# Kernel tuning notes

Hardware: AMD Instinct MI355X
Metric: run time of the kernel (lower is better)

Reference implementation:

```python
import jax, jax.numpy as jnp
import numpy as np

EPS = 1e-6

def layernorm2d(x, w, b):
    # normalize over channel dim (axis=1) of NCHW, per spatial location
    mu = jnp.mean(x, axis=1, keepdims=True)
    var = jnp.var(x, axis=1, keepdims=True)
    xn = (x - mu) * jax.lax.rsqrt(var + EPS)
    return xn * w[None, :, None, None] + b[None, :, None, None]

def conv1x1(x, w, b):
    # x: (B,C,H,W), w: (O,C), b: (O,)
    return jnp.einsum('bchw,oc->bohw', x, w) + b[None, :, None, None]

def setup_inputs() -> dict:
    key = jax.random.key(0)
    ks = jax.random.split(key, 9)
    B, C, H, W = 8, 256, 128, 128
    scale = 1.0 / np.sqrt(C)
    return {
        'x': jax.random.normal(ks[0], (B, C, H, W), jnp.float32),
        'norm_w': jnp.ones((C,), jnp.float32),
        'norm_b': jnp.zeros((C,), jnp.float32),
        'wq': jax.random.normal(ks[1], (C, C), jnp.float32) * scale,
        'bq': jnp.zeros((C,), jnp.float32),
        'wk': jax.random.normal(ks[2], (C, C), jnp.float32) * scale,
        'bk': jnp.zeros((C,), jnp.float32),
        'wv': jax.random.normal(ks[3], (C, C), jnp.float32) * scale,
        'bv': jnp.zeros((C,), jnp.float32),
        'beta': jax.random.normal(ks[4], (1, C, 1, 1), jnp.float32) * 0.1,
    }

def reference(x, norm_w, norm_b, wq, bq, wk, bk, wv, bv, beta):
    C = x.shape[1]
    scale = C ** (-0.5)
    xn = layernorm2d(x, norm_w, norm_b)
    Q = conv1x1(xn, wq, bq)          # (B,C,H,W)
    K = conv1x1(xn, wk, bk)          # (B,C,H,W)
    V = conv1x1(x, wv, bv)           # (B,C,H,W)
    # axial (per-row) attention: logits (B,H,W,W)
    attn = jnp.einsum('bchw,bchv->bhwv', Q, K) * scale
    A = jax.nn.softmax(attn, axis=-1)
    F_self = jnp.einsum('bhwv,bchv->bchw', A, V)
    return x + F_self * beta
```

## Files before the change

### kernel.cpp

```cpp
#include <hip/hip_runtime.h>
#include <hip/hip_bf16.h>

typedef short short8 __attribute__((ext_vector_type(8)));
typedef float f32x4 __attribute__((ext_vector_type(4)));

#define LDS_BYTES 163840
#define XS 0
#define XN 65536
#define AT 65536
#define YT 98304
#define GB 131072
#define SUMSO 139264
#define SQSO 141312
#define MUO 143360
#define RSO 143872
#define UDO 144384

__device__ inline unsigned short cvtbf(float f){
  unsigned int x = __float_as_uint(f);
  x += 0x7fffu + ((x >> 16) & 1u);
  return (unsigned short)(x >> 16);
}
__device__ inline float bf2f(unsigned short u){ return __uint_as_float(((unsigned int)u) << 16); }
__device__ inline unsigned int pk2(float a, float b){ return (unsigned int)cvtbf(a) | ((unsigned int)cvtbf(b) << 16); }

__global__ void __launch_bounds__(256) setup_kernel(
    const float* __restrict__ wq, const float* __restrict__ bq,
    const float* __restrict__ wk, const float* __restrict__ wvw,
    unsigned short* __restrict__ Mbf, unsigned short* __restrict__ wvbf, float* __restrict__ u){
  int c1 = blockIdx.x, t = threadIdx.x;
  float acc = 0.f;
  for (int o = 0; o < 256; ++o) acc = fmaf(wq[o*256 + c1], wk[o*256 + t], acc);
  Mbf[c1*256 + t] = cvtbf(acc);
  wvbf[c1*256 + t] = cvtbf(wvw[c1*256 + t]);
  if (c1 == 0){
    float a2 = 0.f;
    for (int o = 0; o < 256; ++o) a2 = fmaf(wk[o*256 + t], bq[o], a2);
    u[t] = a2;
  }
}

__global__ void __launch_bounds__(512, 2) fused_kernel(
    const float* __restrict__ x, const float* __restrict__ nw, const float* __restrict__ nb,
    const float* __restrict__ bvv, const float* __restrict__ beta,
    const unsigned short* __restrict__ Mbf, const unsigned short* __restrict__ wvbf,
    const float* __restrict__ u, float* __restrict__ out){
  extern __shared__ char smem[];
  const int t = threadIdx.x;
  const int lane = t & 63, wv8 = t >> 6;
  const int g = lane >> 4, li = lane & 15;
  const int blk = blockIdx.x;
  const int b = blk >> 7, h = blk & 127;
  const size_t base = (size_t)b*4194304 + (size_t)h*128;

  #pragma unroll
  for (int i = 0; i < 16; ++i){
    int f = t + i*512;
    int c = f >> 5, w4 = f & 31;
    const float4 v = *(const float4*)(x + base + (size_t)c*16384 + (size_t)(w4*4));
    uint2 p; p.x = pk2(v.x, v.y); p.y = pk2(v.z, v.w);
    *(uint2*)(smem + XS + c*256 + ((w4*8) ^ ((c&7)<<4))) = p;
  }
  __syncthreads();

  {
    int w = t & 127, s = t >> 7;
    float sm = 0.f, sq = 0.f;
    for (int j = 0; j < 64; ++j){
      int c = s*64 + j;
      float xv = bf2f(*(const unsigned short*)(smem + XS + c*256 + ((2*w) ^ ((c&7)<<4))));
      sm += xv; sq += xv*xv;
    }
    ((float*)(smem + SUMSO))[s*128 + w] = sm;
    ((float*)(smem + SQSO))[s*128 + w] = sq;
  }
  __syncthreads();
  if (t < 128){
    float sm = 0.f, sq = 0.f;
    for (int s = 0; s < 4; ++s){ sm += ((float*)(smem+SUMSO))[s*128+t]; sq += ((float*)(smem+SQSO))[s*128+t]; }
    float mu = sm * (1.f/256.f);
    float var = sq * (1.f/256.f) - mu*mu;
    ((float*)(smem+MUO))[t] = mu;
    ((float*)(smem+RSO))[t] = rsqrtf(var + 1e-6f);
  }
  __syncthreads();

  {
    int w = t & 127, s = t >> 7;
    float mu = ((float*)(smem+MUO))[w], rs = ((float*)(smem+RSO))[w];
    float ud = 0.f;
    for (int i = 0; i < 8; ++i){
      int c0 = s*64 + i*8;
      short8 o8;
      #pragma unroll
      for (int j = 0; j < 8; ++j){
        int c = c0 + j;
        float xv = bf2f(*(const unsigned short*)(smem + XS + c*256 + ((2*w) ^ ((c&7)<<4))));
        float xnv = (xv - mu)*rs*nw[c] + nb[c];
        o8[j] = (short)cvtbf(xnv);
        ud = fmaf(u[c], xnv, ud);
      }
      *(short8*)(smem + XN + w*512 + ((2*c0) ^ ((w&7)<<4))) = o8;
    }
    ((float*)(smem+SUMSO))[s*128 + w] = ud;
  }
  __syncthreads();
  if (t < 128){
    float ud = 0.f; for (int s = 0; s < 4; ++s) ud += ((float*)(smem+SUMSO))[s*128+t];
    ((float*)(smem+UDO))[t] = ud;
  }
  __syncthreads();

  f32x4 Sacc[8];
  #pragma unroll
  for (int vt = 0; vt < 8; ++vt){
    int vb = vt*16 + g*4;
    #pragma unroll
    for (int r = 0; r < 4; ++r) Sacc[vt][r] = ((float*)(smem+UDO))[vb + r];
  }
  const int ot = wv8 >> 2, vp = wv8 & 3;
  const int wt = wv8;
  for (int k8 = 0; k8 < 8; ++k8){
    f32x4 Ga[2] = {{0.f,0.f,0.f,0.f},{0.f,0.f,0.f,0.f}};
    #pragma unroll
    for (int kk = 0; kk < 8; ++kk){
      int o = k8*32 + ot*16 + li;
      short8 afr = *(const short8*)(Mbf + o*256 + kk*32 + g*8);
      #pragma unroll
      for (int j = 0; j < 2; ++j){
        int v = (vp*2 + j)*16 + li;
        short8 bfr = *(const short8*)(smem + XN + v*512 + ((2*(kk*32 + g*8)) ^ ((v&7)<<4)));
        Ga[j] = __builtin_amdgcn_mfma_f32_16x16x32_bf16(afr, bfr, Ga[j], 0, 0, 0);
      }
    }
    __syncthreads();
    #pragma unroll
    for (int j = 0; j < 2; ++j){
      int v = (vp*2 + j)*16 + li;
      int ob = ot*16 + g*4;
      uint2 p; p.x = pk2(Ga[j][0], Ga[j][1]); p.y = pk2(Ga[j][2], Ga[j][3]);
      *(uint2*)(smem + GB + v*64 + ((2*ob) ^ ((v&3)<<4))) = p;
    }
    __syncthreads();
    {
      int w = wt*16 + li;
      short8 bfr = *(const short8*)(smem + XN + w*512 + ((2*(k8*32 + g*8)) ^ ((w&7)<<4)));
      #pragma unroll
      for (int vt = 0; vt < 8; ++vt){
        int v = vt*16 + li;
        short8 afr = *(const short8*)(smem + GB + v*64 + ((16*g) ^ ((v&3)<<4)));
        Sacc[vt] = __builtin_amdgcn_mfma_f32_16x16x32_bf16(afr, bfr, Sacc[vt], 0, 0, 0);
      }
    }
  }
  __syncthreads();

  float mx = -3.4e38f;
  #pragma unroll
  for (int vt = 0; vt < 8; ++vt)
    #pragma unroll
    for (int r = 0; r < 4; ++r){ float sv = Sacc[vt][r]*0.0625f; Sacc[vt][r] = sv; mx = fmaxf(mx, sv); }
  mx = fmaxf(mx, __shfl_xor(mx, 16));
  mx = fmaxf(mx, __shfl_xor(mx, 32));
  float sum = 0.f;
  #pragma unroll
  for (int vt = 0; vt < 8; ++vt)
    #pragma unroll
    for (int r = 0; r < 4; ++r){ float p = exp2f((Sacc[vt][r]-mx)*1.44269504f); Sacc[vt][r] = p; sum += p; }
  sum += __shfl_xor(sum, 16);
  sum += __shfl_xor(sum, 32);
  float inv = 1.f / sum;
  {
    int w = wt*16 + li;
    #pragma unroll
    for (int vt = 0; vt < 8; ++vt){
      uint2 p; p.x = pk2(Sacc[vt][0]*inv, Sacc[vt][1]*inv); p.y = pk2(Sacc[vt][2]*inv, Sacc[vt][3]*inv);
      int vb = vt*16 + g*4;
      *(uint2*)(smem + AT + w*256 + ((2*vb) ^ ((w&7)<<4))) = p;
    }
  }
  __syncthreads();

  f32x4 Yacc[2][8];
  #pragma unroll
  for (int ci = 0; ci < 2; ++ci)
    #pragma unroll
    for (int w2 = 0; w2 < 8; ++w2) Yacc[ci][w2] = (f32x4){0.f,0.f,0.f,0.f};
  #pragma unroll
  for (int kk = 0; kk < 4; ++kk){
    short8 afr[2];
    #pragma unroll
    for (int ci = 0; ci < 2; ++ci){
      int c = (wv8*2 + ci)*16 + li;
      afr[ci] = *(const short8*)(smem + XS + c*256 + ((2*(kk*32 + g*8)) ^ ((c&7)<<4)));
    }
    #pragma unroll
    for (int w2 = 0; w2 < 8; ++w2){
      int w = w2*16 + li;
      short8 bfr = *(const short8*)(smem + AT + w*256 + ((2*(kk*32 + g*8)) ^ ((w&7)<<4)));
      #pragma unroll
      for (int ci = 0; ci < 2; ++ci)
        Yacc[ci][w2] = __builtin_amdgcn_mfma_f32_16x16x32_bf16(afr[ci], bfr, Yacc[ci][w2], 0, 0, 0);
    }
  }
  #pragma unroll
  for (int ci = 0; ci < 2; ++ci){
    int cb = (wv8*2 + ci)*16 + g*4;
    #pragma unroll
    for (int w2 = 0; w2 < 8; ++w2){
      int w = w2*16 + li;
      uint2 p; p.x = pk2(Yacc[ci][w2][0], Yacc[ci][w2][1]); p.y = pk2(Yacc[ci][w2][2], Yacc[ci][w2][3]);
      *(uint2*)(smem + YT + w*512 + ((2*cb) ^ ((w&7)<<4))) = p;
    }
  }
  __syncthreads();

  f32x4 Facc[2][8];
  #pragma unroll
  for (int oi = 0; oi < 2; ++oi)
    #pragma unroll
    for (int w2 = 0; w2 < 8; ++w2) Facc[oi][w2] = (f32x4){0.f,0.f,0.f,0.f};
  #pragma unroll
  for (int kk = 0; kk < 8; ++kk){
    short8 afr[2];
    #pragma unroll
    for (int oi = 0; oi < 2; ++oi){
      int o = (wv8*2 + oi)*16 + li;
      afr[oi] = *(const short8*)(wvbf + o*256 + kk*32 + g*8);
    }
    #pragma unroll
    for (int w2 = 0; w2 < 8; ++w2){
      int w = w2*16 + li;
      short8 bfr = *(const short8*)(smem + YT + w*512 + ((2*(kk*32 + g*8)) ^ ((w&7)<<4)));
      #pragma unroll
      for (int oi = 0; oi < 2; ++oi)
        Facc[oi][w2] = __builtin_amdgcn_mfma_f32_16x16x32_bf16(afr[oi], bfr, Facc[oi][w2], 0, 0, 0);
    }
  }
  #pragma unroll
  for (int oi = 0; oi < 2; ++oi){
    #pragma unroll
    for (int r = 0; r < 4; ++r){
      int o = (wv8*2 + oi)*16 + g*4 + r;
      float bvo = bvv[o], bto = beta[o];
      #pragma unroll
      for (int w2 = 0; w2 < 8; ++w2){
        int w = w2*16 + li;
        size_t idx = base + (size_t)o*16384 + (size_t)w;
        out[idx] = x[idx] + (Facc[oi][w2][r] + bvo)*bto;
      }
    }
  }
}

extern "C" void kernel_launch(void* const* d_in, const int* in_sizes, int n_in,
                              void* d_out, int out_size, void* d_ws, size_t ws_size,
                              hipStream_t stream) {
  (void)in_sizes; (void)n_in; (void)out_size; (void)ws_size;
  const float* x      = (const float*)d_in[0];
  const float* norm_w = (const float*)d_in[1];
  const float* norm_b = (const float*)d_in[2];
  const float* wq     = (const float*)d_in[3];
  const float* bq     = (const float*)d_in[4];
  const float* wk     = (const float*)d_in[5];
  const float* wvw    = (const float*)d_in[7];
  const float* bvv    = (const float*)d_in[8];
  const float* beta   = (const float*)d_in[9];
  float* out = (float*)d_out;

  unsigned short* Mbf  = (unsigned short*)d_ws;
  unsigned short* wvbf = (unsigned short*)((char*)d_ws + 131072);
  float* u             = (float*)((char*)d_ws + 262144);

  static bool attr_set = false;
  if (!attr_set) {
    (void)hipFuncSetAttribute((const void*)fused_kernel,
                              hipFuncAttributeMaxDynamicSharedMemorySize, LDS_BYTES);
    attr_set = true;
  }

  setup_kernel<<<256, 256, 0, stream>>>(wq, bq, wk, wvw, Mbf, wvbf, u);
  fused_kernel<<<1024, 512, LDS_BYTES, stream>>>(x, norm_w, norm_b, bvv, beta, Mbf, wvbf, u, out);
}
```

Measured before the change: 192.1 us.

## Shrink LDS footprint by dropping x tile and splitting Y staging in halves

Removes the bf16 copy of x from shared memory: layernorm statistics are computed straight from global loads, with x kept in registers as packed bf16, and the V-projection operand is reloaded from global/L2 and converted on the fly. The Y intermediate is staged in two channel halves that reuse a smaller buffer, cutting LDS from about 160KB to about 78KB. Launch bounds are raised to allow 4 blocks per CU. The setup kernel now computes four rows per block. The cost is higher register pressure (32 packed registers plus the accumulators), repeated global reads of x, and extra barriers from the two-half staging.

```diff
diff --git a/kernel.cpp b/kernel.cpp
--- a/kernel.cpp
+++ b/kernel.cpp
@@ -4,17 +4,16 @@
 typedef short short8 __attribute__((ext_vector_type(8)));
 typedef float f32x4 __attribute__((ext_vector_type(4)));
 
-#define LDS_BYTES 163840
-#define XS 0
-#define XN 65536
-#define AT 65536
-#define YT 98304
-#define GB 131072
-#define SUMSO 139264
-#define SQSO 141312
-#define MUO 143360
-#define RSO 143872
-#define UDO 144384
+#define XN 0
+#define AT 0
+#define YTH 32768
+#define GB 65536
+#define SUMO 73728
+#define SQO 75776
+#define MUO 77824
+#define RSO 78336
+#define UDO 78848
+#define LDS_BYTES 79360
 
 __device__ inline unsigned short cvtbf(float f){
   unsigned int x = __float_as_uint(f);
@@ -28,20 +27,28 @@
     const float* __restrict__ wq, const float* __restrict__ bq,
     const float* __restrict__ wk, const float* __restrict__ wvw,
     unsigned short* __restrict__ Mbf, unsigned short* __restrict__ wvbf, float* __restrict__ u){
-  int c1 = blockIdx.x, t = threadIdx.x;
-  float acc = 0.f;
-  for (int o = 0; o < 256; ++o) acc = fmaf(wq[o*256 + c1], wk[o*256 + t], acc);
-  Mbf[c1*256 + t] = cvtbf(acc);
-  wvbf[c1*256 + t] = cvtbf(wvw[c1*256 + t]);
-  if (c1 == 0){
+  int t = threadIdx.x;
+  int c1b = blockIdx.x * 4;
+  float acc[4] = {0.f,0.f,0.f,0.f};
+  for (int o = 0; o < 256; ++o){
+    float wkv = wk[o*256 + t];
+    #pragma unroll
+    for (int i = 0; i < 4; ++i) acc[i] = fmaf(wq[o*256 + c1b + i], wkv, acc[i]);
+  }
+  #pragma unroll
+  for (int i = 0; i < 4; ++i){
+    Mbf[(c1b+i)*256 + t] = cvtbf(acc[i]);
+    wvbf[(c1b+i)*256 + t] = cvtbf(wvw[(c1b+i)*256 + t]);
+  }
+  if (blockIdx.x == 0){
     float a2 = 0.f;
     for (int o = 0; o < 256; ++o) a2 = fmaf(wk[o*256 + t], bq[o], a2);
     u[t] = a2;
   }
 }
 
-__global__ void __launch_bounds__(512, 2) fused_kernel(
-    const float* __restrict__ x, const float* __restrict__ nw, const float* __restrict__ nb,
+__global__ void __launch_bounds__(512, 4) fused_kernel(
+    const float* __restrict__ x, const float* __restrict__ nw, const float* __restrict__ nbp,
     const float* __restrict__ bvv, const float* __restrict__ beta,
     const unsigned short* __restrict__ Mbf, const unsigned short* __restrict__ wvbf,
     const float* __restrict__ u, float* __restrict__ out){
@@ -53,31 +60,26 @@
   const int b = blk >> 7, h = blk & 127;
   const size_t base = (size_t)b*4194304 + (size_t)h*128;
 
-  #pragma unroll
-  for (int i = 0; i < 16; ++i){
-    int f = t + i*512;
-    int c = f >> 5, w4 = f & 31;
-    const float4 v = *(const float4*)(x + base + (size_t)c*16384 + (size_t)(w4*4));
-    uint2 p; p.x = pk2(v.x, v.y); p.y = pk2(v.z, v.w);
-    *(uint2*)(smem + XS + c*256 + ((w4*8) ^ ((c&7)<<4))) = p;
-  }
-  __syncthreads();
-
+  const int w = t & 127, s = t >> 7;
+  unsigned int xp[32];
   {
-    int w = t & 127, s = t >> 7;
+    const float* xw = x + base + (size_t)(s*64)*16384 + w;
     float sm = 0.f, sq = 0.f;
-    for (int j = 0; j < 64; ++j){
-      int c = s*64 + j;
-      float xv = bf2f(*(const unsigned short*)(smem + XS + c*256 + ((2*w) ^ ((c&7)<<4))));
-      sm += xv; sq += xv*xv;
-    }
-    ((float*)(smem + SUMSO))[s*128 + w] = sm;
-    ((float*)(smem + SQSO))[s*128 + w] = sq;
+    #pragma unroll
+    for (int j = 0; j < 32; ++j){
+      float a0 = xw[(size_t)(2*j)*16384];
+      float a1 = xw[(size_t)(2*j+1)*16384];
+      sm += a0 + a1;
+      sq = fmaf(a0, a0, sq); sq = fmaf(a1, a1, sq);
+      xp[j] = pk2(a0, a1);
+    }
+    ((float*)(smem + SUMO))[s*128 + w] = sm;
+    ((float*)(smem + SQO))[s*128 + w] = sq;
   }
   __syncthreads();
   if (t < 128){
     float sm = 0.f, sq = 0.f;
-    for (int s = 0; s < 4; ++s){ sm += ((float*)(smem+SUMSO))[s*128+t]; sq += ((float*)(smem+SQSO))[s*128+t]; }
+    for (int q = 0; q < 4; ++q){ sm += ((float*)(smem+SUMO))[q*128+t]; sq += ((float*)(smem+SQO))[q*128+t]; }
     float mu = sm * (1.f/256.f);
     float var = sq * (1.f/256.f) - mu*mu;
     ((float*)(smem+MUO))[t] = mu;
@@ -86,27 +88,31 @@
   __syncthreads();
 
   {
-    int w = t & 127, s = t >> 7;
     float mu = ((float*)(smem+MUO))[w], rs = ((float*)(smem+RSO))[w];
     float ud = 0.f;
+    #pragma unroll
     for (int i = 0; i < 8; ++i){
       int c0 = s*64 + i*8;
       short8 o8;
       #pragma unroll
-      for (int j = 0; j < 8; ++j){
-        int c = c0 + j;
-        float xv = bf2f(*(const unsigned short*)(smem + XS + c*256 + ((2*w) ^ ((c&7)<<4))));
-        float xnv = (xv - mu)*rs*nw[c] + nb[c];
-        o8[j] = (short)cvtbf(xnv);
-        ud = fmaf(u[c], xnv, ud);
+      for (int j = 0; j < 4; ++j){
+        unsigned int p = xp[i*4 + j];
+        int c = c0 + j*2;
+        float xa = bf2f((unsigned short)(p & 0xffffu));
+        float xb = bf2f((unsigned short)(p >> 16));
+        float na = (xa - mu)*rs*nw[c]   + nbp[c];
+        float nbv = (xb - mu)*rs*nw[c+1] + nbp[c+1];
+        ud = fmaf(u[c], na, fmaf(u[c+1], nbv, ud));
+        o8[j*2]   = (short)cvtbf(na);
+        o8[j*2+1] = (short)cvtbf(nbv);
       }
       *(short8*)(smem + XN + w*512 + ((2*c0) ^ ((w&7)<<4))) = o8;
     }
-    ((float*)(smem+SUMSO))[s*128 + w] = ud;
+    ((float*)(smem+SUMO))[s*128 + w] = ud;
   }
   __syncthreads();
   if (t < 128){
-    float ud = 0.f; for (int s = 0; s < 4; ++s) ud += ((float*)(smem+SUMSO))[s*128+t];
+    float ud = 0.f; for (int q = 0; q < 4; ++q) ud += ((float*)(smem+SUMO))[q*128+t];
     ((float*)(smem+UDO))[t] = ud;
   }
   __syncthreads();
@@ -143,8 +149,8 @@
     }
     __syncthreads();
     {
-      int w = wt*16 + li;
-      short8 bfr = *(const short8*)(smem + XN + w*512 + ((2*(k8*32 + g*8)) ^ ((w&7)<<4)));
+      int ww = wt*16 + li;
+      short8 bfr = *(const short8*)(smem + XN + ww*512 + ((2*(k8*32 + g*8)) ^ ((ww&7)<<4)));
       #pragma unroll
       for (int vt = 0; vt < 8; ++vt){
         int v = vt*16 + li;
@@ -171,12 +177,12 @@
   sum += __shfl_xor(sum, 32);
   float inv = 1.f / sum;
   {
-    int w = wt*16 + li;
+    int ww = wt*16 + li;
     #pragma unroll
     for (int vt = 0; vt < 8; ++vt){
       uint2 p; p.x = pk2(Sacc[vt][0]*inv, Sacc[vt][1]*inv); p.y = pk2(Sacc[vt][2]*inv, Sacc[vt][3]*inv);
       int vb = vt*16 + g*4;
-      *(uint2*)(smem + AT + w*256 + ((2*vb) ^ ((w&7)<<4))) = p;
+      *(uint2*)(smem + AT + ww*256 + ((2*vb) ^ ((ww&7)<<4))) = p;
     }
   }
   __syncthreads();
@@ -192,51 +198,63 @@
     #pragma unroll
     for (int ci = 0; ci < 2; ++ci){
       int c = (wv8*2 + ci)*16 + li;
-      afr[ci] = *(const short8*)(smem + XS + c*256 + ((2*(kk*32 + g*8)) ^ ((c&7)<<4)));
+      const float* xs = x + base + (size_t)c*16384 + (kk*32 + g*8);
+      const float4 f0 = *(const float4*)xs;
+      const float4 f1 = *(const float4*)(xs + 4);
+      short8 a;
+      a[0]=(short)cvtbf(f0.x); a[1]=(short)cvtbf(f0.y); a[2]=(short)cvtbf(f0.z); a[3]=(short)cvtbf(f0.w);
+      a[4]=(short)cvtbf(f1.x); a[5]=(short)cvtbf(f1.y); a[6]=(short)cvtbf(f1.z); a[7]=(short)cvtbf(f1.w);
+      afr[ci] = a;
     }
     #pragma unroll
     for (int w2 = 0; w2 < 8; ++w2){
-      int w = w2*16 + li;
-      short8 bfr = *(const short8*)(smem + AT + w*256 + ((2*(kk*32 + g*8)) ^ ((w&7)<<4)));
+      int ww = w2*16 + li;
+      short8 bfr = *(const short8*)(smem + AT + ww*256 + ((2*(kk*32 + g*8)) ^ ((ww&7)<<4)));
       #pragma unroll
       for (int ci = 0; ci < 2; ++ci)
         Yacc[ci][w2] = __builtin_amdgcn_mfma_f32_16x16x32_bf16(afr[ci], bfr, Yacc[ci][w2], 0, 0, 0);
     }
   }
-  #pragma unroll
-  for (int ci = 0; ci < 2; ++ci){
-    int cb = (wv8*2 + ci)*16 + g*4;
-    #pragma unroll
-    for (int w2 = 0; w2 < 8; ++w2){
-      int w = w2*16 + li;
-      uint2 p; p.x = pk2(Yacc[ci][w2][0], Yacc[ci][w2][1]); p.y = pk2(Yacc[ci][w2][2], Yacc[ci][w2][3]);
-      *(uint2*)(smem + YT + w*512 + ((2*cb) ^ ((w&7)<<4))) = p;
-    }
-  }
-  __syncthreads();
 
   f32x4 Facc[2][8];
   #pragma unroll
   for (int oi = 0; oi < 2; ++oi)
     #pragma unroll
     for (int w2 = 0; w2 < 8; ++w2) Facc[oi][w2] = (f32x4){0.f,0.f,0.f,0.f};
-  #pragma unroll
-  for (int kk = 0; kk < 8; ++kk){
-    short8 afr[2];
-    #pragma unroll
-    for (int oi = 0; oi < 2; ++oi){
-      int o = (wv8*2 + oi)*16 + li;
-      afr[oi] = *(const short8*)(wvbf + o*256 + kk*32 + g*8);
-    }
-    #pragma unroll
-    for (int w2 = 0; w2 < 8; ++w2){
-      int w = w2*16 + li;
-      short8 bfr = *(const short8*)(smem + YT + w*512 + ((2*(kk*32 + g*8)) ^ ((w&7)<<4)));
-      #pragma unroll
-      for (int oi = 0; oi < 2; ++oi)
-        Facc[oi][w2] = __builtin_amdgcn_mfma_f32_16x16x32_bf16(afr[oi], bfr, Facc[oi][w2], 0, 0, 0);
-    }
-  }
+  for (int half = 0; half < 2; ++half){
+    if ((wv8 >> 2) == half){
+      #pragma unroll
+      for (int ci = 0; ci < 2; ++ci){
+        int cb = ((wv8 & 3)*2 + ci)*16 + g*4;
+        #pragma unroll
+        for (int w2 = 0; w2 < 8; ++w2){
+          int ww = w2*16 + li;
+          uint2 p; p.x = pk2(Yacc[ci][w2][0], Yacc[ci][w2][1]); p.y = pk2(Yacc[ci][w2][2], Yacc[ci][w2][3]);
+          *(uint2*)(smem + YTH + ww*256 + ((2*cb) ^ ((ww&7)<<4))) = p;
+        }
+      }
+    }
+    __syncthreads();
+    #pragma unroll
+    for (int kk = 0; kk < 4; ++kk){
+      short8 afr[2];
+      #pragma unroll
+      for (int oi = 0; oi < 2; ++oi){
+        int o = (wv8*2 + oi)*16 + li;
+        afr[oi] = *(const short8*)(wvbf + o*256 + half*128 + kk*32 + g*8);
+      }
+      #pragma unroll
+      for (int w2 = 0; w2 < 8; ++w2){
+        int ww = w2*16 + li;
+        short8 bfr = *(const short8*)(smem + YTH + ww*256 + ((2*(kk*32 + g*8)) ^ ((ww&7)<<4)));
+        #pragma unroll
+        for (int oi = 0; oi < 2; ++oi)
+          Facc[oi][w2] = __builtin_amdgcn_mfma_f32_16x16x32_bf16(afr[oi], bfr, Facc[oi][w2], 0, 0, 0);
+      }
+    }
+    __syncthreads();
+  }
+
   #pragma unroll
   for (int oi = 0; oi < 2; ++oi){
     #pragma unroll
@@ -245,8 +263,8 @@
       float bvo = bvv[o], bto = beta[o];
       #pragma unroll
       for (int w2 = 0; w2 < 8; ++w2){
-        int w = w2*16 + li;
-        size_t idx = base + (size_t)o*16384 + (size_t)w;
+        int ww = w2*16 + li;
+        size_t idx = base + (size_t)o*16384 + (size_t)ww;
         out[idx] = x[idx] + (Facc[oi][w2][r] + bvo)*bto;
       }
     }
@@ -279,6 +297,6 @@
     attr_set = true;
   }
 
-  setup_kernel<<<256, 256, 0, stream>>>(wq, bq, wk, wvw, Mbf, wvbf, u);
+  setup_kernel<<<64, 256, 0, stream>>>(wq, bq, wk, wvw, Mbf, wvbf, u);
   fused_kernel<<<1024, 512, LDS_BYTES, stream>>>(x, norm_w, norm_b, bvv, beta, Mbf, wvbf, u, out);
 }
```

New measurement: 235.5 us. 22.5% more time.
